# Kernel tuning notes

Hardware: AMD Instinct MI355X
Metric: run time of the kernel (lower is better)

The kernel has to match this reference:

```python
import jax, jax.numpy as jnp
import numpy as np

DIM = 1024
N_HEADS = 16
HEAD_DIM = DIM // N_HEADS
MAX_SEQ = 2048
B, S = 4, 2048


def _rope_tables(seq_len):
    inv_freq = 1.0 / (10000.0 ** (jnp.arange(0, HEAD_DIM, 2, dtype=jnp.float32) / HEAD_DIM))
    t = jnp.arange(seq_len, dtype=jnp.float32)
    freqs = jnp.outer(t, inv_freq)            # [S, HEAD_DIM/2]
    emb = jnp.concatenate([freqs, freqs], -1)  # [S, HEAD_DIM]
    return jnp.cos(emb), jnp.sin(emb)


def _apply_rope(x, cos, sin):
    # x: [B, S, H, Dh]; cos/sin: [S, Dh]
    c = cos[None, :, None, :]
    s = sin[None, :, None, :]
    x1, x2 = jnp.split(x, 2, axis=-1)
    x_rot = jnp.concatenate([-x2, x1], -1)
    return x * c + x_rot * s


def setup_inputs() -> dict:
    key = jax.random.key(0)
    kx, kq, kk, kv, ko = jax.random.split(key, 5)
    std = DIM ** -0.5
    x = jax.random.normal(kx, (B, S, DIM), jnp.float32)
    Wq = jax.random.normal(kq, (DIM, DIM), jnp.float32) * std
    Wk = jax.random.normal(kk, (DIM, DIM), jnp.float32) * std
    Wv = jax.random.normal(kv, (DIM, DIM), jnp.float32) * std
    Wo = jax.random.normal(ko, (DIM, DIM), jnp.float32) * std
    # causal mask: 1 where attending is allowed, 0 where masked (mask==0 -> -inf)
    mask = jnp.tril(jnp.ones((S, S), jnp.int32))[None, None]  # [1,1,S,S]
    return {"x": x, "Wq": Wq, "Wk": Wk, "Wv": Wv, "Wo": Wo, "mask": mask}


def reference(x, Wq, Wk, Wv, Wo, mask) -> jnp.ndarray:
    b, s, _ = x.shape
    scale = HEAD_DIM ** -0.5
    # torch Linear: y = x @ W.T, W is [out, in]
    q = (x @ Wq.T).reshape(b, s, N_HEADS, HEAD_DIM)
    k = (x @ Wk.T).reshape(b, s, N_HEADS, HEAD_DIM)
    v = (x @ Wv.T).reshape(b, s, N_HEADS, HEAD_DIM)
    cos, sin = _rope_tables(s)
    q = _apply_rope(q, cos, sin)
    k = _apply_rope(k, cos, sin)
    # [B, H, S, S]
    attn = jnp.einsum('bqhd,bkhd->bhqk', q, k) * scale
    attn = jnp.where(mask == 0, -jnp.inf, attn)
    attn = jax.nn.softmax(attn, axis=-1)
    out = jnp.einsum('bhqk,bkhd->bqhd', attn, v).reshape(b, s, DIM)
    return out @ Wo.T
```

## Files before the change

### kernel.cpp

```cpp
#include <hip/hip_runtime.h>
#include <hip/hip_bf16.h>
#include <math.h>

using bf16 = __hip_bfloat16;
typedef __attribute__((ext_vector_type(8))) short short8;
typedef __attribute__((ext_vector_type(4))) float float4v;

#define DIM 1024
#define NH 16
#define HD 64
#define BB 4
#define SS 2048
#define MTOT (BB * SS)

#define ROPE_LOG2 0.41524101186092034f
#define PC1 0.18033688f
#define PC0 -23.08312066f

__device__ inline short bf16bits(float x) {
  return __builtin_bit_cast(short, __float2bfloat16(x));
}
__device__ inline float bits2f(unsigned short b) {
  return __builtin_bit_cast(float, (unsigned)b << 16);
}
__device__ inline unsigned pack2(float a, float b) {
  return (unsigned)(unsigned short)bf16bits(a) |
         ((unsigned)(unsigned short)bf16bits(b) << 16);
}

__device__ inline void async16(const void* g, void* l) {
  __builtin_amdgcn_global_load_lds(
      (const __attribute__((address_space(1))) void*)g,
      (__attribute__((address_space(3))) void*)l, 16, 0, 0);
}

__device__ inline void cvt8(const float* __restrict__ in, bf16* __restrict__ out,
                            size_t i) {
  const float4v* p = (const float4v*)in + i * 2;
  float4v a = p[0], b = p[1];
  short8 r;
  r[0] = bf16bits(a[0]); r[1] = bf16bits(a[1]);
  r[2] = bf16bits(a[2]); r[3] = bf16bits(a[3]);
  r[4] = bf16bits(b[0]); r[5] = bf16bits(b[1]);
  r[6] = bf16bits(b[2]); r[7] = bf16bits(b[3]);
  ((short8*)out)[i] = r;
}

__global__ __launch_bounds__(256) void prep(
    const float* __restrict__ x, const float* __restrict__ w0,
    const float* __restrict__ w1, const float* __restrict__ w2,
    const float* __restrict__ w3, bf16* __restrict__ xb, bf16* __restrict__ o0,
    bf16* __restrict__ o1, bf16* __restrict__ o2, bf16* __restrict__ o3,
    unsigned* __restrict__ tab) {
  const int bid = blockIdx.x;
  const int tid = threadIdx.x;
  if (bid < 4096) {
    cvt8(x, xb, (size_t)bid * 256 + tid);
  } else if (bid < 6144) {
    int wsel = (bid - 4096) >> 9;
    const float* in = wsel == 0 ? w0 : wsel == 1 ? w1 : wsel == 2 ? w2 : w3;
    bf16* out = wsel == 0 ? o0 : wsel == 1 ? o1 : wsel == 2 ? o2 : o3;
    cvt8(in, out, (size_t)((bid - 4096) & 511) * 256 + tid);
  } else {
    int i = (bid - 6144) * 256 + tid;
    int s = i >> 5, d = i & 31;
    float inv = exp2f(-(float)d * ROPE_LOG2);
    float sn, cs;
    sincosf((float)s * inv, &sn, &cs);
    tab[i] = pack2(cs, sn);
  }
}

__global__ __launch_bounds__(256, 3) void gemm_qkv(
    const bf16* __restrict__ A, const bf16* __restrict__ W,
    bf16* __restrict__ Cbase, const unsigned* __restrict__ rt) {
  __shared__ __align__(16) short sPool[4][4096];
  short* sT = &sPool[0][0];

  const int tid = threadIdx.x;
  const int wave = tid >> 6;
  const int lane = tid & 63;
  const int l15 = lane & 15;
  const int quad = lane >> 4;
  const int m0 = blockIdx.x * 128;
  const int n0 = blockIdx.y * 128;
  const int wm = (wave >> 1) * 64;
  const int wn = (wave & 1) * 64;
  const int K = DIM;

  float4v acc[4][4];
#pragma unroll
  for (int i = 0; i < 4; i++)
#pragma unroll
    for (int j = 0; j < 4; j++)
#pragma unroll
      for (int r = 0; r < 4; r++) acc[i][j][r] = 0.0f;

  auto stage = [&](int buf, int k0) {
    short* dA = &sPool[buf * 2][0];
    short* dB = &sPool[buf * 2 + 1][0];
#pragma unroll
    for (int i = 0; i < 2; i++) {
      int c0 = i * 256 + wave * 64;
      int c = c0 + lane;
      int row = c >> 2, cb = c & 3;
      async16(A + (size_t)(m0 + row) * K + k0 + cb * 8, dA + c0 * 8);
      async16(W + (size_t)(n0 + row) * K + k0 + cb * 8, dB + c0 * 8);
    }
  };

  stage(0, 0);
  __syncthreads();

  int cur = 0;
  for (int k0 = 0; k0 < K; k0 += 32, cur ^= 1) {
    if (k0 + 32 < K) stage(cur ^ 1, k0 + 32);

    const short* sA = &sPool[cur * 2][0];
    const short* sB = &sPool[cur * 2 + 1][0];
    short8 af[4], bfr[4];
#pragma unroll
    for (int mi = 0; mi < 4; mi++)
      af[mi] = *(const short8*)(sA + (wm + mi * 16 + l15) * 32 + quad * 8);
#pragma unroll
    for (int ni = 0; ni < 4; ni++)
      bfr[ni] = *(const short8*)(sB + (wn + ni * 16 + l15) * 32 + quad * 8);
#pragma unroll
    for (int mi = 0; mi < 4; mi++)
#pragma unroll
      for (int ni = 0; ni < 4; ni++)
        acc[mi][ni] = __builtin_amdgcn_mfma_f32_16x16x32_bf16(
            af[mi], bfr[ni], acc[mi][ni], 0, 0, 0);

    __syncthreads();
  }

  const int third = n0 >> 10;
  const int nloc = n0 & 1023;
  bf16* C = Cbase + (size_t)third * MTOT * DIM;

  if (third == 2) {
    const int bb_ = m0 >> 11;
    const int s0 = m0 & (SS - 1);
    const int h0 = nloc >> 6;
#pragma unroll
    for (int half = 0; half < 2; half++) {
      if (half) __syncthreads();
      if ((wave & 1) == half) {
#pragma unroll
        for (int mi = 0; mi < 4; mi++)
#pragma unroll
          for (int ni = 0; ni < 4; ni++)
#pragma unroll
            for (int r = 0; r < 4; r++)
              sT[(ni * 16 + l15) * 130 + wm + mi * 16 + quad * 4 + r] =
                  bf16bits(acc[mi][ni][r]);
      }
      __syncthreads();
      int row = tid >> 2, cb = tid & 3;
      size_t base =
          ((size_t)(bb_ * NH + h0 + half) * HD + row) * SS + s0 + cb * 32;
#pragma unroll
      for (int c = 0; c < 4; c++) {
        short8 vv = *(const short8*)(sT + row * 130 + cb * 32 + c * 8);
        *(short8*)((short*)C + base + c * 8) = vv;
      }
    }
    return;
  }

#pragma unroll
  for (int mi = 0; mi < 4; mi++) {
#pragma unroll
    for (int r = 0; r < 4; r++) {
      int m = m0 + wm + mi * 16 + quad * 4 + r;
      int b = m >> 11;
      int s = m & (SS - 1);
      int h = (nloc + wn) >> 6;
      bf16* outp = C + ((size_t)(b * NH + h) * SS + s) * HD;
#pragma unroll
      for (int ni = 0; ni < 2; ni++) {
        int d = ni * 16 + l15;
        unsigned cspack = rt[s * 32 + d];
        float cs = bits2f((unsigned short)(cspack & 0xffff));
        float sn = bits2f((unsigned short)(cspack >> 16));
        float lo = acc[mi][ni][r];
        float hi = acc[mi][ni + 2][r];
        outp[d] = __float2bfloat16(lo * cs - hi * sn);
        outp[d + 32] = __float2bfloat16(hi * cs + lo * sn);
      }
    }
  }
}

__global__ __launch_bounds__(256, 3) void gemm_out(const bf16* __restrict__ A,
                                                   const bf16* __restrict__ W,
                                                   float* __restrict__ C) {
  __shared__ __align__(16) short sPool[4][4096];

  const int tid = threadIdx.x;
  const int wave = tid >> 6;
  const int lane = tid & 63;
  const int l15 = lane & 15;
  const int quad = lane >> 4;
  const int m0 = blockIdx.x * 128;
  const int n0 = blockIdx.y * 128;
  const int wm = (wave >> 1) * 64;
  const int wn = (wave & 1) * 64;
  const int K = DIM, N = DIM;

  float4v acc[4][4];
#pragma unroll
  for (int i = 0; i < 4; i++)
#pragma unroll
    for (int j = 0; j < 4; j++)
#pragma unroll
      for (int r = 0; r < 4; r++) acc[i][j][r] = 0.0f;

  auto stage = [&](int buf, int k0) {
    short* dA = &sPool[buf * 2][0];
    short* dB = &sPool[buf * 2 + 1][0];
#pragma unroll
    for (int i = 0; i < 2; i++) {
      int c0 = i * 256 + wave * 64;
      int c = c0 + lane;
      int row = c >> 2, cb = c & 3;
      async16(A + (size_t)(m0 + row) * K + k0 + cb * 8, dA + c0 * 8);
      async16(W + (size_t)(n0 + row) * K + k0 + cb * 8, dB + c0 * 8);
    }
  };

  stage(0, 0);
  __syncthreads();

  int cur = 0;
  for (int k0 = 0; k0 < K; k0 += 32, cur ^= 1) {
    if (k0 + 32 < K) stage(cur ^ 1, k0 + 32);

    const short* sA = &sPool[cur * 2][0];
    const short* sB = &sPool[cur * 2 + 1][0];
    short8 af[4], bfr[4];
#pragma unroll
    for (int mi = 0; mi < 4; mi++)
      af[mi] = *(const short8*)(sA + (wm + mi * 16 + l15) * 32 + quad * 8);
#pragma unroll
    for (int ni = 0; ni < 4; ni++)
      bfr[ni] = *(const short8*)(sB + (wn + ni * 16 + l15) * 32 + quad * 8);
#pragma unroll
    for (int mi = 0; mi < 4; mi++)
#pragma unroll
      for (int ni = 0; ni < 4; ni++)
        acc[mi][ni] = __builtin_amdgcn_mfma_f32_16x16x32_bf16(
            af[mi], bfr[ni], acc[mi][ni], 0, 0, 0);

    __syncthreads();
  }

#pragma unroll
  for (int mi = 0; mi < 4; mi++) {
#pragma unroll
    for (int r = 0; r < 4; r++) {
      int m = m0 + wm + mi * 16 + quad * 4 + r;
#pragma unroll
      for (int ni = 0; ni < 4; ni++) {
        int n = n0 + wn + ni * 16 + l15;
        C[(size_t)m * N + n] = acc[mi][ni][r];
      }
    }
  }
}

#define SKV 64
#define SP 64

__global__ __launch_bounds__(256, 2) void attn_fwd(const bf16* __restrict__ q,
                                                   const bf16* __restrict__ k,
                                                   const bf16* __restrict__ vt,
                                                   bf16* __restrict__ o) {
  __shared__ __align__(16) short sK[2][64 * SKV];
  __shared__ __align__(16) short sV[2][64 * SKV];
  __shared__ __align__(16) short sP[4][16 * SP];

  const int tid = threadIdx.x;
  const int wave = tid >> 6;
  const int lane = tid & 63;
  const int l15 = lane & 15;
  const int quad = lane >> 4;
  const int bh = blockIdx.x;
  const int p = blockIdx.y;
  const int qt[4] = {p, 15 - p, 16 + p, 31 - p};
  const size_t hb = (size_t)bh * SS * HD;
  const size_t vtb = (size_t)bh * HD * SS;

  short8 aQ[4][2];
#pragma unroll
  for (int ti = 0; ti < 4; ti++) {
    const bf16* qp =
        q + hb + (size_t)(qt[ti] * 64 + wave * 16 + l15) * HD + quad * 8;
    aQ[ti][0] = *(const short8*)qp;
    aQ[ti][1] = *(const short8*)(qp + 32);
  }

  float l_part[4] = {0.0f, 0.0f, 0.0f, 0.0f};
  float4v acc_o[4][4];
#pragma unroll
  for (int ti = 0; ti < 4; ti++)
#pragma unroll
    for (int di = 0; di < 4; di++)
#pragma unroll
      for (int r = 0; r < 4; r++) acc_o[ti][di][r] = 0.0f;

  int4 kr[2], vr[2];
  auto load_kv = [&](int kt_) {
    int k0n = kt_ * 64;
#pragma unroll
    for (int i = 0; i < 2; i++) {
      int c = tid + i * 256;
      kr[i] = *(const int4*)(k + hb + (size_t)(k0n + (c >> 3)) * HD + (c & 7) * 8);
      vr[i] = *(const int4*)(vt + vtb + (size_t)(c >> 3) * SS + k0n + (c & 7) * 8);
    }
  };
  auto stage_write = [&](int buf) {
#pragma unroll
    for (int i = 0; i < 2; i++) {
      int c = tid + i * 256;
      int row = c >> 3;
      int sl = (c & 7) ^ (row & 7);
      *(int4*)(&sK[buf][row * SKV + sl * 8]) = kr[i];
      *(int4*)(&sV[buf][row * SKV + sl * 8]) = vr[i];
    }
  };

  load_kv(0);
  stage_write(0);
  __syncthreads();

  const int maxkt = qt[3];
  for (int kt = 0; kt <= maxkt; kt++) {
    const int cur = kt & 1;
    if (kt < maxkt) load_kv(kt + 1);

    short8 kf[8], vf[8];
#pragma unroll
    for (int t = 0; t < 2; t++)
#pragma unroll
      for (int i = 0; i < 4; i++) {
        int row = i * 16 + l15;
        int sl = (t * 4 + quad) ^ (l15 & 7);
        kf[t * 4 + i] = *(const short8*)(&sK[cur][row * SKV + sl * 8]);
        vf[t * 4 + i] = *(const short8*)(&sV[cur][row * SKV + sl * 8]);
      }

    const int k0 = kt * 64;
    short* pw = &sP[wave][0];
#pragma unroll
    for (int ti = 0; ti < 4; ti++) {
      if (kt <= qt[ti]) {
        float4v s[4];
#pragma unroll
        for (int ni = 0; ni < 4; ni++)
#pragma unroll
          for (int r = 0; r < 4; r++) s[ni][r] = 0.0f;
        __builtin_amdgcn_s_setprio(1);
#pragma unroll
        for (int t = 0; t < 2; t++)
#pragma unroll
          for (int ni = 0; ni < 4; ni++)
            s[ni] = __builtin_amdgcn_mfma_f32_16x16x32_bf16(
                kf[t * 4 + ni], aQ[ti][t], s[ni], 0, 0, 0);
        __builtin_amdgcn_s_setprio(0);

        const bool diag = (kt == qt[ti]);
        const int qglob = qt[ti] * 64 + wave * 16 + l15;
#pragma unroll
        for (int ni = 0; ni < 4; ni++) {
          float pe[4];
#pragma unroll
          for (int r = 0; r < 4; r++) {
            float x = exp2f(fmaf(s[ni][r], PC1, PC0));
            if (diag && (k0 + ni * 16 + quad * 4 + r > qglob)) x = 0.0f;
            l_part[ti] += x;
            pe[r] = x;
          }
          int2 w2;
          w2.x = (int)pack2(pe[0], pe[1]);
          w2.y = (int)pack2(pe[2], pe[3]);
          int slw = (2 * ni + (quad >> 1)) ^ (l15 & 7);
          *(int2*)(pw + l15 * SP + slw * 8 + (quad & 1) * 4) = w2;
        }
        asm volatile("s_waitcnt lgkmcnt(0)" ::: "memory");

        __builtin_amdgcn_s_setprio(1);
#pragma unroll
        for (int t = 0; t < 2; t++) {
          int slr = (t * 4 + quad) ^ (l15 & 7);
          short8 aP = *(const short8*)(pw + l15 * SP + slr * 8);
#pragma unroll
          for (int di = 0; di < 4; di++)
            acc_o[ti][di] = __builtin_amdgcn_mfma_f32_16x16x32_bf16(
                aP, vf[t * 4 + di], acc_o[ti][di], 0, 0, 0);
        }
        __builtin_amdgcn_s_setprio(0);
      }
    }

    if (kt < maxkt) stage_write(cur ^ 1);
    __syncthreads();
  }

  const int b = bh >> 4, h = bh & 15;
#pragma unroll
  for (int ti = 0; ti < 4; ti++) {
    float lr = l_part[ti];
    lr += __shfl_xor(lr, 16, 64);
    lr += __shfl_xor(lr, 32, 64);
#pragma unroll
    for (int r = 0; r < 4; r++) {
      float invl = 1.0f / __shfl(lr, quad * 4 + r, 64);
      bf16* op =
          o + (size_t)(b * SS + qt[ti] * 64 + wave * 16 + quad * 4 + r) * DIM +
          h * HD;
#pragma unroll
      for (int di = 0; di < 4; di++)
        op[di * 16 + l15] = __float2bfloat16(acc_o[ti][di][r] * invl);
    }
  }
}

extern "C" void kernel_launch(void* const* d_in, const int* in_sizes, int n_in,
                              void* d_out, int out_size, void* d_ws,
                              size_t ws_size, hipStream_t stream) {
  const float* x = (const float*)d_in[0];
  const float* Wq = (const float*)d_in[1];
  const float* Wk = (const float*)d_in[2];
  const float* Wv = (const float*)d_in[3];
  const float* Wo = (const float*)d_in[4];
  float* out = (float*)d_out;

  char* ws = (char*)d_ws;
  const size_t xsz = (size_t)MTOT * DIM * sizeof(bf16);
  bf16* xb = (bf16*)ws;
  bf16* qb_ = (bf16*)(ws + xsz);
  bf16* kb = (bf16*)(ws + 2 * xsz);
  bf16* vtb = (bf16*)(ws + 3 * xsz);
  bf16* wqb = (bf16*)(ws + 4 * xsz);
  bf16* wkb = wqb + (size_t)DIM * DIM;
  bf16* wvb = wkb + (size_t)DIM * DIM;
  bf16* wob = wvb + (size_t)DIM * DIM;
  unsigned* rt = (unsigned*)(wob + (size_t)DIM * DIM);
  bf16* ob = xb;

  dim3 bb(256);
  prep<<<dim3(6400), bb, 0, stream>>>(x, Wq, Wk, Wv, Wo, xb, wqb, wkb, wvb,
                                      wob, rt);
  gemm_qkv<<<dim3(MTOT / 128, 3 * DIM / 128), bb, 0, stream>>>(xb, wqb, qb_,
                                                               rt);
  attn_fwd<<<dim3(BB * NH, 8), bb, 0, stream>>>(qb_, kb, vtb, ob);
  gemm_out<<<dim3(MTOT / 128, DIM / 128), bb, 0, stream>>>(ob, wob, out);
}
```

Baseline: 288.7 us.

## Merge two causal query-tile groups per block to share K/V staging

The attention kernel now runs 512 threads as two 4-wave groups. Each group owns a different balanced set of four query tiles (p-based and 7-p-based pairings), and both share one K/V tile stream loaded into LDS. This halves the grid in y and halves the redundant K/V global loads per head, since each thread loads one chunk instead of two. In exchange, blocks are larger, the loop runs to the max of both groups, so the inactive group idles on some tiles, and occupancy may drop under the 512-thread launch bound.

```diff
diff --git a/kernel.cpp b/kernel.cpp
--- a/kernel.cpp
+++ b/kernel.cpp
@@ -273,22 +273,26 @@
 #define SKV 64
 #define SP 64
 
-__global__ __launch_bounds__(256, 2) void attn_fwd(const bf16* __restrict__ q,
+__global__ __launch_bounds__(512, 2) void attn_fwd(const bf16* __restrict__ q,
                                                    const bf16* __restrict__ k,
                                                    const bf16* __restrict__ vt,
                                                    bf16* __restrict__ o) {
   __shared__ __align__(16) short sK[2][64 * SKV];
   __shared__ __align__(16) short sV[2][64 * SKV];
-  __shared__ __align__(16) short sP[4][16 * SP];
+  __shared__ __align__(16) short sP[8][16 * SP];
 
   const int tid = threadIdx.x;
   const int wave = tid >> 6;
+  const int g = wave >> 2;
+  const int wv = wave & 3;
   const int lane = tid & 63;
   const int l15 = lane & 15;
   const int quad = lane >> 4;
   const int bh = blockIdx.x;
   const int p = blockIdx.y;
-  const int qt[4] = {p, 15 - p, 16 + p, 31 - p};
+  const int qt[4] = {g == 0 ? p : 7 - p, g == 0 ? 15 - p : 8 + p,
+                     g == 0 ? 16 + p : 23 - p, g == 0 ? 31 - p : 24 + p};
+  const int maxkt = 31 - p;
   const size_t hb = (size_t)bh * SS * HD;
   const size_t vtb = (size_t)bh * HD * SS;
 
@@ -296,7 +300,7 @@
 #pragma unroll
   for (int ti = 0; ti < 4; ti++) {
     const bf16* qp =
-        q + hb + (size_t)(qt[ti] * 64 + wave * 16 + l15) * HD + quad * 8;
+        q + hb + (size_t)(qt[ti] * 64 + wv * 16 + l15) * HD + quad * 8;
     aQ[ti][0] = *(const short8*)qp;
     aQ[ti][1] = *(const short8*)(qp + 32);
   }
@@ -310,32 +314,25 @@
 #pragma unroll
       for (int r = 0; r < 4; r++) acc_o[ti][di][r] = 0.0f;
 
-  int4 kr[2], vr[2];
+  int4 kr, vr;
   auto load_kv = [&](int kt_) {
     int k0n = kt_ * 64;
-#pragma unroll
-    for (int i = 0; i < 2; i++) {
-      int c = tid + i * 256;
-      kr[i] = *(const int4*)(k + hb + (size_t)(k0n + (c >> 3)) * HD + (c & 7) * 8);
-      vr[i] = *(const int4*)(vt + vtb + (size_t)(c >> 3) * SS + k0n + (c & 7) * 8);
-    }
+    int c = tid;
+    kr = *(const int4*)(k + hb + (size_t)(k0n + (c >> 3)) * HD + (c & 7) * 8);
+    vr = *(const int4*)(vt + vtb + (size_t)(c >> 3) * SS + k0n + (c & 7) * 8);
   };
   auto stage_write = [&](int buf) {
-#pragma unroll
-    for (int i = 0; i < 2; i++) {
-      int c = tid + i * 256;
-      int row = c >> 3;
-      int sl = (c & 7) ^ (row & 7);
-      *(int4*)(&sK[buf][row * SKV + sl * 8]) = kr[i];
-      *(int4*)(&sV[buf][row * SKV + sl * 8]) = vr[i];
-    }
+    int c = tid;
+    int row = c >> 3;
+    int sl = (c & 7) ^ (row & 7);
+    *(int4*)(&sK[buf][row * SKV + sl * 8]) = kr;
+    *(int4*)(&sV[buf][row * SKV + sl * 8]) = vr;
   };
 
   load_kv(0);
   stage_write(0);
   __syncthreads();
 
-  const int maxkt = qt[3];
   for (int kt = 0; kt <= maxkt; kt++) {
     const int cur = kt & 1;
     if (kt < maxkt) load_kv(kt + 1);
@@ -371,7 +368,7 @@
         __builtin_amdgcn_s_setprio(0);
 
         const bool diag = (kt == qt[ti]);
-        const int qglob = qt[ti] * 64 + wave * 16 + l15;
+        const int qglob = qt[ti] * 64 + wv * 16 + l15;
 #pragma unroll
         for (int ni = 0; ni < 4; ni++) {
           float pe[4];
@@ -418,7 +415,7 @@
     for (int r = 0; r < 4; r++) {
       float invl = 1.0f / __shfl(lr, quad * 4 + r, 64);
       bf16* op =
-          o + (size_t)(b * SS + qt[ti] * 64 + wave * 16 + quad * 4 + r) * DIM +
+          o + (size_t)(b * SS + qt[ti] * 64 + wv * 16 + quad * 4 + r) * DIM +
           h * HD;
 #pragma unroll
       for (int di = 0; di < 4; di++)
@@ -455,6 +452,6 @@
                                       wob, rt);
   gemm_qkv<<<dim3(MTOT / 128, 3 * DIM / 128), bb, 0, stream>>>(xb, wqb, qb_,
                                                                rt);
-  attn_fwd<<<dim3(BB * NH, 8), bb, 0, stream>>>(qb_, kb, vtb, ob);
+  attn_fwd<<<dim3(BB * NH, 4), dim3(512), 0, stream>>>(qb_, kb, vtb, ob);
   gemm_out<<<dim3(MTOT / 128, DIM / 128), bb, 0, stream>>>(ob, wob, out);
 }
```

Measured after the change: 269.4 us. 6.7% less time.
